# Optimization experiments

Measured on AMD Instinct MI355X. Metric: run time of the kernel, lower is better.

## Reference

```python
import jax, jax.numpy as jnp
import numpy as np

NUM_HEADS = 4  # nn.MultiheadAttention(num_heads=4)


def setup_inputs() -> dict:
    key = jax.random.key(0)
    ks = jax.random.split(key, 9)
    E, D, B, S = 16, 128, 8, 512
    H2 = D // 2
    s = 0.05
    return {
        "lstm_features": jax.random.normal(ks[0], (B, S, D), dtype=jnp.float32),
        "Wqkv": jax.random.normal(ks[1], (E, 3 * D, D), dtype=jnp.float32) * s,
        "bqkv": jax.random.normal(ks[2], (E, 3 * D), dtype=jnp.float32) * s,
        "Wo": jax.random.normal(ks[3], (E, D, D), dtype=jnp.float32) * s,
        "bo": jax.random.normal(ks[4], (E, D), dtype=jnp.float32) * s,
        "W1": jax.random.normal(ks[5], (E, H2, D), dtype=jnp.float32) * s,
        "b1": jax.random.normal(ks[6], (E, H2), dtype=jnp.float32) * s,
        "W2": jax.random.normal(ks[7], (E, 1, H2), dtype=jnp.float32) * s,
        "b2": jax.random.normal(ks[8], (E, 1), dtype=jnp.float32) * s,
    }


def reference(lstm_features, Wqkv, bqkv, Wo, bo, W1, b1, W2, b2):
    # lstm_features: [B, S, D]; params stacked over E=num_events.
    B, S, D = lstm_features.shape
    E = Wqkv.shape[0]
    H = NUM_HEADS
    Dh = D // H

    # Grouped in-projection for all events at once: [E, B, S, 3D]
    qkv = jnp.einsum("bsd,ekd->ebsk", lstm_features, Wqkv) + bqkv[:, None, None, :]
    q, k, v = jnp.split(qkv, 3, axis=-1)  # each [E, B, S, D]

    def heads(t):  # [E,B,S,D] -> [E,B,H,S,Dh]
        return t.reshape(E, B, S, H, Dh).transpose(0, 1, 3, 2, 4)

    q, k, v = heads(q), heads(k), heads(v)

    scale = 1.0 / jnp.sqrt(jnp.asarray(Dh, dtype=lstm_features.dtype))
    scores = jnp.einsum("ebhqd,ebhkd->ebhqk", q, k) * scale  # [E,B,H,S,S]
    attn = jax.nn.softmax(scores, axis=-1)
    ctx = jnp.einsum("ebhqk,ebhkd->ebhqd", attn, v)  # [E,B,H,S,Dh]
    ctx = ctx.transpose(0, 1, 3, 2, 4).reshape(E, B, S, D)

    attended = jnp.einsum("ebsd,eod->ebso", ctx, Wo) + bo[:, None, None, :]

    # Per-event MLP head: D -> D//2 -> 1 (dropout is identity in eval)
    h = jax.nn.relu(jnp.einsum("ebsd,ehd->ebsh", attended, W1) + b1[:, None, None, :])
    logits = jnp.einsum("ebsh,eoh->ebso", h, W2) + b2[:, None, None, :]  # [E,B,S,1]
    logits = logits[..., 0]  # [E,B,S]

    # torch.stack(..., dim=2) -> [B, S, E]
    return logits.transpose(1, 2, 0)
```

## Files before the change

### kernel.cpp

```cpp
#include <hip/hip_runtime.h>
#include <hip/hip_bf16.h>


#define E_ 16
#define B_ 8
#define S_ 512
#define D_ 128
#define H_ 4
#define DH_ 32
#define H2_ 64
#define M_ (B_ * S_)
#define QK_SCALE_L2E 0.25503472437616588f

#define ATTN_LDS_BYTES (512 * 80 + 32 * 1040)
#define HEAD_LDS_BYTES (128 * 136 * 2 * 2)
#define QKV_LDS_BYTES  (128 * 136 * 2 * 2)

typedef __attribute__((ext_vector_type(4))) short bf16x4;
typedef __attribute__((ext_vector_type(8))) short bf16x8;
typedef __attribute__((ext_vector_type(4))) float f32x4;

__device__ __forceinline__ short f2bf(float f) {
    unsigned u = __builtin_bit_cast(unsigned, f);
    u += 0x7fffu + ((u >> 16) & 1u);
    return (short)(u >> 16);
}

__device__ __forceinline__ unsigned pk2(float lo, float hi) {
    __hip_bfloat162 t = __float22bfloat162_rn(make_float2(lo, hi));
    unsigned r;
    __builtin_memcpy(&r, &t, sizeof(r));
    return r;
}

__device__ __forceinline__ bf16x8 cat8(bf16x4 lo, bf16x4 hi) {
    return __builtin_shufflevector(lo, hi, 0, 1, 2, 3, 4, 5, 6, 7);
}

__global__ __launch_bounds__(256) void convert_kernel(
    const float* __restrict__ x, const float* __restrict__ w,
    const float* __restrict__ wo, const float* __restrict__ w1,
    short* __restrict__ xbf, short* __restrict__ wbf,
    short* __restrict__ wobf, short* __restrict__ w1bf)
{
    const int XN  = (M_ * D_) / 8;
    const int WN  = (E_ * 3 * D_ * D_) / 8;
    const int WON = (E_ * D_ * D_) / 8;
    const int W1N = (E_ * H2_ * D_) / 8;
    int idx = blockIdx.x * 256 + threadIdx.x;
    const float* src; short* dst; int off;
    if (idx < XN)                        { src = x;  dst = xbf;  off = idx; }
    else if (idx < XN + WN)              { src = w;  dst = wbf;  off = idx - XN; }
    else if (idx < XN + WN + WON)        { src = wo; dst = wobf; off = idx - XN - WN; }
    else if (idx < XN + WN + WON + W1N)  { src = w1; dst = w1bf; off = idx - XN - WN - WON; }
    else return;
    float4 v0 = *(const float4*)&src[(size_t)off * 8];
    float4 v1 = *(const float4*)&src[(size_t)off * 8 + 4];
    bf16x8 o;
    o[0] = f2bf(v0.x); o[1] = f2bf(v0.y); o[2] = f2bf(v0.z); o[3] = f2bf(v0.w);
    o[4] = f2bf(v1.x); o[5] = f2bf(v1.y); o[6] = f2bf(v1.z); o[7] = f2bf(v1.w);
    *(bf16x8*)&dst[(size_t)off * 8] = o;
}

__global__ __launch_bounds__(512) void qkv_mfma_kernel(
    const short* __restrict__ xbf,
    const short* __restrict__ wbf,
    const float* __restrict__ bqkv,
    short* __restrict__ q, short* __restrict__ k, short* __restrict__ v)
{
    extern __shared__ __align__(16) char lds[];
    short (*xs)[136] = (short(*)[136])lds;
    short (*ws)[136] = (short(*)[136])(lds + 128 * 136 * 2);

    const int ct2 = blockIdx.x;
    const int rt  = blockIdx.y;
    const int e   = blockIdx.z;
    const int tid = threadIdx.x;
    const int w    = tid >> 6;
    const int lane = tid & 63;
    const int l15  = lane & 15;
    const int g    = lane >> 4;

    #pragma unroll
    for (int p = 0; p < 4; ++p) {
        int idx = tid + p * 512;
        int row = idx >> 4, c8 = (idx & 15) * 8;
        *(bf16x8*)&xs[row][c8] =
            *(const bf16x8*)&xbf[(size_t)(rt * 128 + row) * 128 + c8];
        *(bf16x8*)&ws[row][c8] =
            *(const bf16x8*)&wbf[((size_t)e * 384 + ct2 * 128 + row) * 128 + c8];
    }
    __syncthreads();

    const int m0 = (w >> 2) * 64;
    const int n0 = (w & 3) * 32;
    f32x4 acc[4][2] = {};

    #pragma unroll
    for (int kk = 0; kk < 128; kk += 32) {
        bf16x8 A0 = *(const bf16x8*)&ws[n0      + l15][kk + 8 * g];
        bf16x8 A1 = *(const bf16x8*)&ws[n0 + 16 + l15][kk + 8 * g];
        #pragma unroll
        for (int mm = 0; mm < 4; ++mm) {
            bf16x8 Bm = *(const bf16x8*)&xs[m0 + mm * 16 + l15][kk + 8 * g];
            acc[mm][0] = __builtin_amdgcn_mfma_f32_16x16x32_bf16(A0, Bm, acc[mm][0], 0, 0, 0);
            acc[mm][1] = __builtin_amdgcn_mfma_f32_16x16x32_bf16(A1, Bm, acc[mm][1], 0, 0, 0);
        }
    }

    if (ct2 < 2) {
        short* dst = (ct2 == 0) ? q : k;
        const float scale = (ct2 == 0) ? QK_SCALE_L2E : 1.0f;
        #pragma unroll
        for (int mm = 0; mm < 4; ++mm) {
            #pragma unroll
            for (int nn = 0; nn < 2; ++nn) {
                const int d  = n0 + nn * 16 + 4 * g;
                const int h  = d >> 5, dh = d & 31;
                const int jb = ct2 * 128 + d;
                const float b0 = bqkv[e * 384 + jb + 0];
                const float b1 = bqkv[e * 384 + jb + 1];
                const float b2 = bqkv[e * 384 + jb + 2];
                const float b3 = bqkv[e * 384 + jb + 3];
                const int m  = rt * 128 + m0 + mm * 16 + l15;
                const int bb = m >> 9, s = m & 511;
                bf16x4 o;
                o[0] = f2bf((acc[mm][nn][0] + b0) * scale);
                o[1] = f2bf((acc[mm][nn][1] + b1) * scale);
                o[2] = f2bf((acc[mm][nn][2] + b2) * scale);
                o[3] = f2bf((acc[mm][nn][3] + b3) * scale);
                *(bf16x4*)&dst[((((size_t)e * B_ + bb) * H_ + h) * S_ + s) * DH_ + dh] = o;
            }
        }
    } else {
        __syncthreads();
        float (*rp)[132] = (float(*)[132])lds;
        #pragma unroll
        for (int mm = 0; mm < 4; ++mm) {
            #pragma unroll
            for (int nn = 0; nn < 2; ++nn) {
                const int jl = n0 + nn * 16 + 4 * g;
                const int ml = m0 + mm * 16 + l15;
                rp[jl + 0][ml] = acc[mm][nn][0];
                rp[jl + 1][ml] = acc[mm][nn][1];
                rp[jl + 2][ml] = acc[mm][nn][2];
                rp[jl + 3][ml] = acc[mm][nn][3];
            }
        }
        __syncthreads();
        const int bb = (rt * 128) >> 9;
        const int sb = (rt * 128) & 511;
        #pragma unroll
        for (int p = 0; p < 4; ++p) {
            int task = tid + p * 512;
            int jl = task >> 4, sc = (task & 15) * 8;
            const int h = jl >> 5, dh = jl & 31;
            const float bias = bqkv[e * 384 + 256 + jl];
            bf16x8 o;
            #pragma unroll
            for (int j = 0; j < 8; ++j) o[j] = f2bf(rp[jl][sc + j] + bias);
            *(bf16x8*)&v[((((size_t)e * B_ + bb) * H_ + h) * DH_ + dh) * S_ + sb + sc] = o;
        }
    }
}

__global__ __launch_bounds__(512) void attn_kernel(
    const short* __restrict__ q, const short* __restrict__ k,
    const short* __restrict__ vt, short* __restrict__ ctxbf)
{
    extern __shared__ __align__(16) char smem[];
    char* Kbase  = smem;
    char* VTbase = smem + 40960;

    const int bh  = blockIdx.x;
    const int e   = blockIdx.y;
    const int tid = threadIdx.x;
    const int w    = tid >> 6;
    const int lane = tid & 63;
    const int l15  = lane & 15;
    const int g    = lane >> 4;

    const size_t base = ((size_t)e * 32 + bh) * (S_ * DH_);
    const short* qg = q  + base;
    const short* kg = k  + base;
    const short* vg = vt + base;

    {
        const uint4* src = (const uint4*)(kg + (size_t)tid * DH_);
        uint4* dst = (uint4*)(Kbase + (size_t)tid * 80);
        dst[0] = src[0]; dst[1] = src[1]; dst[2] = src[2]; dst[3] = src[3];
    }
    {
        int d = tid >> 4, c0 = (tid & 15) * 32;
        const uint4* src = (const uint4*)(vg + (size_t)d * S_ + c0);
        uint4* dst = (uint4*)(VTbase + (size_t)d * 1040 + c0 * 2);
        dst[0] = src[0]; dst[1] = src[1]; dst[2] = src[2]; dst[3] = src[3];
    }
    bf16x8 bq[4];
    #pragma unroll
    for (int qf = 0; qf < 4; ++qf) {
        const short* qp = qg + (size_t)(w * 64 + qf * 16 + l15) * DH_;
        bq[qf] = *(const bf16x8*)(qp + 8 * g);
    }
    __syncthreads();

    bf16x8 ones;
    #pragma unroll
    for (int j = 0; j < 8; ++j) ones[j] = (short)0x3F80;

    f32x4 acc0[4] = {}, acc1[4] = {};
    f32x4 accS[4] = {};

    for (int kt = 0; kt < 16; ++kt) {
        const char* kp = Kbase + (size_t)(kt * 32 + l15) * 80 + g * 16;
        bf16x8 ka0 = *(const bf16x8*)kp;
        bf16x8 ka1 = *(const bf16x8*)(kp + 16 * 80);
        const int keyb = kt * 32;
        const char* vp = VTbase + (size_t)l15 * 1040 + (keyb + 4 * g) * 2;
        bf16x8 va0 = cat8(*(const bf16x4*)vp, *(const bf16x4*)(vp + 32));
        const char* vq = vp + 16 * 1040;
        bf16x8 va1 = cat8(*(const bf16x4*)vq, *(const bf16x4*)(vq + 32));

        #pragma unroll
        for (int qf = 0; qf < 4; ++qf) {
            f32x4 z = {0.f, 0.f, 0.f, 0.f};
            f32x4 s0 = __builtin_amdgcn_mfma_f32_16x16x32_bf16(ka0, bq[qf], z, 0, 0, 0);
            f32x4 s1 = __builtin_amdgcn_mfma_f32_16x16x32_bf16(ka1, bq[qf], z, 0, 0, 0);
            float p0 = __builtin_amdgcn_exp2f(s0[0]);
            float p1 = __builtin_amdgcn_exp2f(s0[1]);
            float p2 = __builtin_amdgcn_exp2f(s0[2]);
            float p3 = __builtin_amdgcn_exp2f(s0[3]);
            float p4 = __builtin_amdgcn_exp2f(s1[0]);
            float p5 = __builtin_amdgcn_exp2f(s1[1]);
            float p6 = __builtin_amdgcn_exp2f(s1[2]);
            float p7 = __builtin_amdgcn_exp2f(s1[3]);
            uint4 uu = make_uint4(pk2(p0, p1), pk2(p2, p3),
                                  pk2(p4, p5), pk2(p6, p7));
            bf16x8 pf = __builtin_bit_cast(bf16x8, uu);
            acc0[qf] = __builtin_amdgcn_mfma_f32_16x16x32_bf16(va0, pf, acc0[qf], 0, 0, 0);
            acc1[qf] = __builtin_amdgcn_mfma_f32_16x16x32_bf16(va1, pf, acc1[qf], 0, 0, 0);
            accS[qf] = __builtin_amdgcn_mfma_f32_16x16x32_bf16(ones, pf, accS[qf], 0, 0, 0);
        }
    }

    const int b = bh >> 2, h = bh & 3;
    #pragma unroll
    for (int qf = 0; qf < 4; ++qf) {
        const float inv = 1.0f / accS[qf][0];
        const int qrow = w * 64 + qf * 16 + l15;
        short* cg = ctxbf + (((size_t)(e * B_ + b) * S_ + qrow) * D_ + h * DH_);
        bf16x4 o0, o1;
        #pragma unroll
        for (int r = 0; r < 4; ++r) {
            o0[r] = f2bf(acc0[qf][r] * inv);
            o1[r] = f2bf(acc1[qf][r] * inv);
        }
        *(bf16x4*)&cg[4 * g]      = o0;
        *(bf16x4*)&cg[16 + 4 * g] = o1;
    }
}

__global__ __launch_bounds__(512) void head_mfma_kernel(
    const short* __restrict__ ctxbf,
    const short* __restrict__ wobf,
    const float* __restrict__ bo,
    const short* __restrict__ w1bf,
    const float* __restrict__ b1,
    const float* __restrict__ W2,
    const float* __restrict__ b2,
    float* __restrict__ out)
{
    extern __shared__ __align__(16) char smem[];
    short (*Wos)[136] = (short(*)[136])smem;
    short (*cts)[136] = (short(*)[136])(smem + 128 * 136 * 2);

    const int mt  = blockIdx.x;
    const int e   = blockIdx.y;
    const int tid = threadIdx.x;
    const int w    = tid >> 6;
    const int lane = tid & 63;
    const int l15  = lane & 15;
    const int g    = lane >> 4;

    #pragma unroll
    for (int p = 0; p < 4; ++p) {
        int idx = tid + p * 512;
        int row = idx >> 4, c8 = (idx & 15) * 8;
        *(bf16x8*)&Wos[row][c8] =
            *(const bf16x8*)&wobf[((size_t)e * 128 + row) * 128 + c8];
        *(bf16x8*)&cts[row][c8] =
            *(const bf16x8*)&ctxbf[((size_t)e * M_ + mt * 128 + row) * 128 + c8];
    }
    __syncthreads();

    f32x4 accA[8] = {};
    #pragma unroll
    for (int kk = 0; kk < 128; kk += 32) {
        bf16x8 a = *(const bf16x8*)&cts[w * 16 + l15][kk + 8 * g];
        #pragma unroll
        for (int t = 0; t < 8; ++t) {
            bf16x8 bfr = *(const bf16x8*)&Wos[t * 16 + l15][kk + 8 * g];
            accA[t] = __builtin_amdgcn_mfma_f32_16x16x32_bf16(a, bfr, accA[t], 0, 0, 0);
        }
    }
    __syncthreads();

    #pragma unroll
    for (int p = 0; p < 2; ++p) {
        int idx = tid + p * 512;
        int row = idx >> 4, c8 = (idx & 15) * 8;
        *(bf16x8*)&Wos[row][c8] =
            *(const bf16x8*)&w1bf[((size_t)e * 64 + row) * 128 + c8];
    }
    #pragma unroll
    for (int t = 0; t < 8; ++t) {
        const float bov = bo[e * 128 + t * 16 + l15];
        #pragma unroll
        for (int r = 0; r < 4; ++r)
            cts[w * 16 + 4 * g + r][t * 16 + l15] = f2bf(accA[t][r] + bov);
    }
    __syncthreads();

    f32x4 accB[4] = {};
    #pragma unroll
    for (int kk = 0; kk < 128; kk += 32) {
        bf16x8 a = *(const bf16x8*)&cts[w * 16 + l15][kk + 8 * g];
        #pragma unroll
        for (int t = 0; t < 4; ++t) {
            bf16x8 bfr = *(const bf16x8*)&Wos[t * 16 + l15][kk + 8 * g];
            accB[t] = __builtin_amdgcn_mfma_f32_16x16x32_bf16(a, bfr, accB[t], 0, 0, 0);
        }
    }

    float b1v[4], w2v[4];
    #pragma unroll
    for (int t = 0; t < 4; ++t) {
        b1v[t] = b1[e * 64 + t * 16 + l15];
        w2v[t] = W2[e * 64 + t * 16 + l15];
    }
    const float b2v = b2[e];
    #pragma unroll
    for (int r = 0; r < 4; ++r) {
        float s = 0.f;
        #pragma unroll
        for (int t = 0; t < 4; ++t)
            s += fmaxf(accB[t][r] + b1v[t], 0.f) * w2v[t];
        s += __shfl_xor(s, 1);
        s += __shfl_xor(s, 2);
        s += __shfl_xor(s, 4);
        s += __shfl_xor(s, 8);
        if (l15 == 0) {
            const int m = mt * 128 + w * 16 + 4 * g + r;
            const int bb = m >> 9, ss = m & 511;
            out[((size_t)(bb * S_ + ss)) * E_ + e] = s + b2v;
        }
    }
}

extern "C" void kernel_launch(void* const* d_in, const int* in_sizes, int n_in,
                              void* d_out, int out_size, void* d_ws, size_t ws_size,
                              hipStream_t stream) {
    const float* x    = (const float*)d_in[0];
    const float* Wqkv = (const float*)d_in[1];
    const float* bqkv = (const float*)d_in[2];
    const float* Wo   = (const float*)d_in[3];
    const float* bo   = (const float*)d_in[4];
    const float* W1   = (const float*)d_in[5];
    const float* b1   = (const float*)d_in[6];
    const float* W2   = (const float*)d_in[7];
    const float* b2   = (const float*)d_in[8];
    float* out = (float*)d_out;

    const size_t SZ = (size_t)E_ * B_ * H_ * S_ * DH_;
    short* qb    = (short*)d_ws;
    short* kb    = qb + SZ;
    short* vtb   = kb + SZ;
    short* ctxbf = vtb + SZ;
    short* xbf   = ctxbf + SZ;
    short* wbf   = xbf + (size_t)M_ * D_;
    short* wobf  = wbf + (size_t)E_ * 3 * D_ * D_;
    short* w1bf  = wobf + (size_t)E_ * D_ * D_;

    hipFuncSetAttribute((const void*)qkv_mfma_kernel,
                        hipFuncAttributeMaxDynamicSharedMemorySize,
                        QKV_LDS_BYTES);
    hipFuncSetAttribute((const void*)attn_kernel,
                        hipFuncAttributeMaxDynamicSharedMemorySize,
                        ATTN_LDS_BYTES);
    hipFuncSetAttribute((const void*)head_mfma_kernel,
                        hipFuncAttributeMaxDynamicSharedMemorySize,
                        HEAD_LDS_BYTES);

    convert_kernel<<<dim3(832), 256, 0, stream>>>(x, Wqkv, Wo, W1, xbf, wbf, wobf, w1bf);
    qkv_mfma_kernel<<<dim3(3, 32, 16), 512, QKV_LDS_BYTES, stream>>>(xbf, wbf, bqkv, qb, kb, vtb);
    attn_kernel<<<dim3(32, 16), 512, ATTN_LDS_BYTES, stream>>>(qb, kb, vtb, ctxbf);
    head_mfma_kernel<<<dim3(32, 16), 512, HEAD_LDS_BYTES, stream>>>(ctxbf, wobf, bo, w1bf, b1, W2, b2, out);
}
```

Baseline: 69.56 us.

## Pre-permute V layout for single 16-byte LDS loads and use packed bf16 conversion

```diff
diff --git a/kernel.cpp b/kernel.cpp
--- a/kernel.cpp
+++ b/kernel.cpp
@@ -31,10 +31,6 @@
     unsigned r;
     __builtin_memcpy(&r, &t, sizeof(r));
     return r;
-}
-
-__device__ __forceinline__ bf16x8 cat8(bf16x4 lo, bf16x4 hi) {
-    return __builtin_shufflevector(lo, hi, 0, 1, 2, 3, 4, 5, 6, 7);
 }
 
 __global__ __launch_bounds__(256) void convert_kernel(
@@ -56,10 +52,9 @@
     else return;
     float4 v0 = *(const float4*)&src[(size_t)off * 8];
     float4 v1 = *(const float4*)&src[(size_t)off * 8 + 4];
-    bf16x8 o;
-    o[0] = f2bf(v0.x); o[1] = f2bf(v0.y); o[2] = f2bf(v0.z); o[3] = f2bf(v0.w);
-    o[4] = f2bf(v1.x); o[5] = f2bf(v1.y); o[6] = f2bf(v1.z); o[7] = f2bf(v1.w);
-    *(bf16x8*)&dst[(size_t)off * 8] = o;
+    uint4 uu = make_uint4(pk2(v0.x, v0.y), pk2(v0.z, v0.w),
+                          pk2(v1.x, v1.y), pk2(v1.z, v1.w));
+    *(uint4*)&dst[(size_t)off * 8] = uu;
 }
 
 __global__ __launch_bounds__(512) void qkv_mfma_kernel(
@@ -124,12 +119,10 @@
                 const float b3 = bqkv[e * 384 + jb + 3];
                 const int m  = rt * 128 + m0 + mm * 16 + l15;
                 const int bb = m >> 9, s = m & 511;
-                bf16x4 o;
-                o[0] = f2bf((acc[mm][nn][0] + b0) * scale);
-                o[1] = f2bf((acc[mm][nn][1] + b1) * scale);
-                o[2] = f2bf((acc[mm][nn][2] + b2) * scale);
-                o[3] = f2bf((acc[mm][nn][3] + b3) * scale);
-                *(bf16x4*)&dst[((((size_t)e * B_ + bb) * H_ + h) * S_ + s) * DH_ + dh] = o;
+                uint2 o = make_uint2(
+                    pk2((acc[mm][nn][0] + b0) * scale, (acc[mm][nn][1] + b1) * scale),
+                    pk2((acc[mm][nn][2] + b2) * scale, (acc[mm][nn][3] + b3) * scale));
+                *(uint2*)&dst[((((size_t)e * B_ + bb) * H_ + h) * S_ + s) * DH_ + dh] = o;
             }
         }
     } else {
@@ -156,10 +149,17 @@
             int jl = task >> 4, sc = (task & 15) * 8;
             const int h = jl >> 5, dh = jl & 31;
             const float bias = bqkv[e * 384 + 256 + jl];
-            bf16x8 o;
+            const int kbase = sc & ~31;
+            const int gq    = (sc >> 3) & 3;
+            float pv[8];
             #pragma unroll
-            for (int j = 0; j < 8; ++j) o[j] = f2bf(rp[jl][sc + j] + bias);
-            *(bf16x8*)&v[((((size_t)e * B_ + bb) * H_ + h) * DH_ + dh) * S_ + sb + sc] = o;
+            for (int j = 0; j < 8; ++j) {
+                const int src_s = kbase + (j >> 2) * 16 + 4 * gq + (j & 3);
+                pv[j] = rp[jl][src_s] + bias;
+            }
+            uint4 o = make_uint4(pk2(pv[0], pv[1]), pk2(pv[2], pv[3]),
+                                 pk2(pv[4], pv[5]), pk2(pv[6], pv[7]));
+            *(uint4*)&v[((((size_t)e * B_ + bb) * H_ + h) * DH_ + dh) * S_ + sb + sc] = o;
         }
     }
 }
@@ -215,11 +215,9 @@
         const char* kp = Kbase + (size_t)(kt * 32 + l15) * 80 + g * 16;
         bf16x8 ka0 = *(const bf16x8*)kp;
         bf16x8 ka1 = *(const bf16x8*)(kp + 16 * 80);
-        const int keyb = kt * 32;
-        const char* vp = VTbase + (size_t)l15 * 1040 + (keyb + 4 * g) * 2;
-        bf16x8 va0 = cat8(*(const bf16x4*)vp, *(const bf16x4*)(vp + 32));
-        const char* vq = vp + 16 * 1040;
-        bf16x8 va1 = cat8(*(const bf16x4*)vq, *(const bf16x4*)(vq + 32));
+        const char* vp = VTbase + (size_t)l15 * 1040 + (size_t)kt * 64 + g * 16;
+        bf16x8 va0 = *(const bf16x8*)vp;
+        bf16x8 va1 = *(const bf16x8*)(vp + 16 * 1040);
 
         #pragma unroll
         for (int qf = 0; qf < 4; ++qf) {
@@ -249,14 +247,12 @@
         const float inv = 1.0f / accS[qf][0];
         const int qrow = w * 64 + qf * 16 + l15;
         short* cg = ctxbf + (((size_t)(e * B_ + b) * S_ + qrow) * D_ + h * DH_);
-        bf16x4 o0, o1;
-        #pragma unroll
-        for (int r = 0; r < 4; ++r) {
-            o0[r] = f2bf(acc0[qf][r] * inv);
-            o1[r] = f2bf(acc1[qf][r] * inv);
-        }
-        *(bf16x4*)&cg[4 * g]      = o0;
-        *(bf16x4*)&cg[16 + 4 * g] = o1;
+        uint2 o0 = make_uint2(pk2(acc0[qf][0] * inv, acc0[qf][1] * inv),
+                              pk2(acc0[qf][2] * inv, acc0[qf][3] * inv));
+        uint2 o1 = make_uint2(pk2(acc1[qf][0] * inv, acc1[qf][1] * inv),
+                              pk2(acc1[qf][2] * inv, acc1[qf][3] * inv));
+        *(uint2*)&cg[4 * g]      = o0;
+        *(uint2*)&cg[16 + 4 * g] = o1;
     }
 }
 
```

Result: no change. 68.98 us, median of 2 (-0.8%).
